# Performance work log

Measured on AMD Instinct MI355X. Metric: run time of the kernel, lower is better.

## Reference

```python
import jax, jax.numpy as jnp
import numpy as np

D_MODEL = 1024
D_FF = 8192
N_ELEM = 64            # d2 (elements per block)
D1 = D_FF // N_ELEM    # 128 block rows
BATCH = 2048


def setup_inputs() -> dict:
    key = jax.random.key(0)
    k1, k2, k3, k4, k5 = jax.random.split(key, 5)
    # xavier-uniform-like init for w1 (d_model, d_ff) -> view (d_model, d1, d2)
    bound1 = float(np.sqrt(6.0 / (D_MODEL + D_FF)))
    w1 = jax.random.uniform(k1, (D_MODEL, D1, N_ELEM), jnp.float32, -bound1, bound1)
    # w2 (d_ff, d_model) -> view (d2, d1, d_model); kernel_scaling=True multiplies by sqrt(d2)
    w2 = jax.random.uniform(k2, (N_ELEM, D1, D_MODEL), jnp.float32, -bound1, bound1)
    w2 = w2 * (N_ELEM ** 0.5)
    b2 = jax.random.normal(k3, (D_MODEL,), jnp.float32)
    x = jax.random.normal(k4, (BATCH, D_MODEL), jnp.float32)
    quant_mask = jax.random.randint(k5, (BATCH, D1), 0, N_ELEM, jnp.int32)
    return {"quant_mask": quant_mask, "x": x, "w1": w1, "w2": w2, "b2": b2}


def reference(quant_mask, x, w1, w2, b2):
    # predict-mode path of SparseFFMain (multiply_by_controller_output=False)
    d1 = w1.shape[1]
    w1p = jnp.transpose(w1, (1, 2, 0))   # (d1, d2, d_model)
    w2p = jnp.transpose(w2, (1, 0, 2))   # (d1, d2, d_model)
    rows = jnp.arange(d1)[None, :]        # (1, d1) broadcasts over batch
    # per-sample gathered expert sub-blocks: (B, d1, d_model)
    w = w1p[rows, quant_mask]
    v = w2p[rows, quant_mask]
    mid = jnp.einsum('bd,bjd->bj', x, w)   # (B, d1)
    relu = jax.nn.relu(mid)
    res = jnp.einsum('bj,bjd->bd', relu, v) + b2  # (B, d_model)
    return (quant_mask, res)
```

## Files before the change

kernel.cpp:

```cpp
#include <hip/hip_runtime.h>

#define D_MODEL 1024
#define D_FF    8192
#define N_ELEM  64
#define D1      128
#define BATCH   2048
#define B_T     8
#define NJT     8
#define JT      16

typedef unsigned short u16;
typedef unsigned int   u32;
typedef _Float16 h2    __attribute__((ext_vector_type(2)));
typedef float    f32x4 __attribute__((ext_vector_type(4)));
typedef u32      u32x2 __attribute__((ext_vector_type(2)));

__device__ __forceinline__ h2 as_h2(u32 u) { union { u32 i; h2 h; } c; c.i = u; return c.h; }
__device__ __forceinline__ u32 pkh(float a, float b) {
    union { h2 h; u32 u; } c; c.h.x = (_Float16)a; c.h.y = (_Float16)b; return c.u;
}
__device__ __forceinline__ u16 f2h(float f) {
    union { _Float16 h; u16 u; } c; c.h = (_Float16)f; return c.u;
}
__device__ __forceinline__ f32x4 ntload4(const float* p) {
    return __builtin_nontemporal_load((const f32x4*)p);
}

__global__ __launch_bounds__(256) void transpose_cast_w1(const float* __restrict__ w1,
                                                         u16* __restrict__ w1h) {
    __shared__ float tile[64][65];
    const int c0 = blockIdx.x * 64;
    const int d0 = blockIdx.y * 64;
    const int tx = threadIdx.x & 15;
    const int ty = threadIdx.x >> 4;
#pragma unroll
    for (int r = 0; r < 4; ++r) {
        const int row = ty * 4 + r;
        const float4 v = *(const float4*)(w1 + (size_t)(d0 + row) * D_FF + c0 + tx * 4);
        tile[row][tx * 4 + 0] = v.x;
        tile[row][tx * 4 + 1] = v.y;
        tile[row][tx * 4 + 2] = v.z;
        tile[row][tx * 4 + 3] = v.w;
    }
    __syncthreads();
#pragma unroll
    for (int r = 0; r < 4; ++r) {
        const int c = ty * 4 + r;
        ushort4 o;
        o.x = f2h(tile[tx * 4 + 0][c]);
        o.y = f2h(tile[tx * 4 + 1][c]);
        o.z = f2h(tile[tx * 4 + 2][c]);
        o.w = f2h(tile[tx * 4 + 3][c]);
        *(ushort4*)(w1h + (size_t)(c0 + c) * D_MODEL + d0 + tx * 4) = o;
    }
}

__global__ __launch_bounds__(256) void cast_w2(const float* __restrict__ w2,
                                               u16* __restrict__ w2h) {
    const size_t i = ((size_t)blockIdx.x * 256 + threadIdx.x) * 8;
    const float4 a = *(const float4*)(w2 + i);
    const float4 b = *(const float4*)(w2 + i + 4);
    ushort4 oa, ob;
    oa.x = f2h(a.x); oa.y = f2h(a.y); oa.z = f2h(a.z); oa.w = f2h(a.w);
    ob.x = f2h(b.x); ob.y = f2h(b.y); ob.z = f2h(b.z); ob.w = f2h(b.w);
    *(ushort4*)(w2h + i)     = oa;
    *(ushort4*)(w2h + i + 4) = ob;
}

__global__ __launch_bounds__(256) void sparse_ff_jt(const int* __restrict__ mask,
                                                    const float* __restrict__ x,
                                                    const u16* __restrict__ w1h_,
                                                    const u16* __restrict__ w2h_,
                                                    u16* __restrict__ part) {
    const _Float16* w1h = (const _Float16*)w1h_;
    const _Float16* w2h = (const _Float16*)w2h_;
    __shared__ u16   x_lds[B_T][D_MODEL];
    __shared__ float r_lds[B_T][JT];
    __shared__ int   m_lds[B_T][JT];

    const int jt = blockIdx.x & (NJT - 1);
    const int b0 = (blockIdx.x >> 3) * B_T;
    const int t = threadIdx.x;
    const int wave = t >> 6;
    const int lane = t & 63;

#pragma unroll
    for (int r = 0; r < B_T; ++r) {
        const f32x4 v = ntload4(x + (size_t)(b0 + r) * D_MODEL + t * 4);
        u32x2 o; o.x = pkh(v.x, v.y); o.y = pkh(v.z, v.w);
        *(u32x2*)&x_lds[r][t * 4] = o;
    }
    if (t < B_T * JT) {
        m_lds[t >> 4][t & 15] = mask[(b0 + (t >> 4)) * D1 + jt * JT + (t & 15)];
    }
    __syncthreads();

#pragma unroll
    for (int rep = 0; rep < 2; ++rep) {
        const int bi = wave * 2 + rep;
        const uint4 xA = *(const uint4*)&x_lds[bi][lane * 8];
        const uint4 xB = *(const uint4*)&x_lds[bi][512 + lane * 8];

        for (int jj = 0; jj < JT; jj += 2) {
            const int j0 = jt * JT + jj;
            const _Float16* c0 = w1h + (size_t)((j0 << 6) + m_lds[bi][jj]) * D_MODEL;
            const _Float16* c1 = w1h + (size_t)(((j0 + 1) << 6) + m_lds[bi][jj + 1]) * D_MODEL;
            const uint4 a0 = *(const uint4*)(c0 + lane * 8);
            const uint4 b0v = *(const uint4*)(c0 + 512 + lane * 8);
            const uint4 a1 = *(const uint4*)(c1 + lane * 8);
            const uint4 b1v = *(const uint4*)(c1 + 512 + lane * 8);

            float s0 = 0.f, s1 = 0.f;
            {
                const h2 w_0 = as_h2(a0.x), w_1 = as_h2(a0.y), w_2 = as_h2(a0.z), w_3 = as_h2(a0.w);
                const h2 q_0 = as_h2(xA.x), q_1 = as_h2(xA.y), q_2 = as_h2(xA.z), q_3 = as_h2(xA.w);
                s0 = fmaf((float)w_0.x, (float)q_0.x, s0); s0 = fmaf((float)w_0.y, (float)q_0.y, s0);
                s0 = fmaf((float)w_1.x, (float)q_1.x, s0); s0 = fmaf((float)w_1.y, (float)q_1.y, s0);
                s0 = fmaf((float)w_2.x, (float)q_2.x, s0); s0 = fmaf((float)w_2.y, (float)q_2.y, s0);
                s0 = fmaf((float)w_3.x, (float)q_3.x, s0); s0 = fmaf((float)w_3.y, (float)q_3.y, s0);
            }
            {
                const h2 w_0 = as_h2(b0v.x), w_1 = as_h2(b0v.y), w_2 = as_h2(b0v.z), w_3 = as_h2(b0v.w);
                const h2 q_0 = as_h2(xB.x), q_1 = as_h2(xB.y), q_2 = as_h2(xB.z), q_3 = as_h2(xB.w);
                s0 = fmaf((float)w_0.x, (float)q_0.x, s0); s0 = fmaf((float)w_0.y, (float)q_0.y, s0);
                s0 = fmaf((float)w_1.x, (float)q_1.x, s0); s0 = fmaf((float)w_1.y, (float)q_1.y, s0);
                s0 = fmaf((float)w_2.x, (float)q_2.x, s0); s0 = fmaf((float)w_2.y, (float)q_2.y, s0);
                s0 = fmaf((float)w_3.x, (float)q_3.x, s0); s0 = fmaf((float)w_3.y, (float)q_3.y, s0);
            }
            {
                const h2 w_0 = as_h2(a1.x), w_1 = as_h2(a1.y), w_2 = as_h2(a1.z), w_3 = as_h2(a1.w);
                const h2 q_0 = as_h2(xA.x), q_1 = as_h2(xA.y), q_2 = as_h2(xA.z), q_3 = as_h2(xA.w);
                s1 = fmaf((float)w_0.x, (float)q_0.x, s1); s1 = fmaf((float)w_0.y, (float)q_0.y, s1);
                s1 = fmaf((float)w_1.x, (float)q_1.x, s1); s1 = fmaf((float)w_1.y, (float)q_1.y, s1);
                s1 = fmaf((float)w_2.x, (float)q_2.x, s1); s1 = fmaf((float)w_2.y, (float)q_2.y, s1);
                s1 = fmaf((float)w_3.x, (float)q_3.x, s1); s1 = fmaf((float)w_3.y, (float)q_3.y, s1);
            }
            {
                const h2 w_0 = as_h2(b1v.x), w_1 = as_h2(b1v.y), w_2 = as_h2(b1v.z), w_3 = as_h2(b1v.w);
                const h2 q_0 = as_h2(xB.x), q_1 = as_h2(xB.y), q_2 = as_h2(xB.z), q_3 = as_h2(xB.w);
                s1 = fmaf((float)w_0.x, (float)q_0.x, s1); s1 = fmaf((float)w_0.y, (float)q_0.y, s1);
                s1 = fmaf((float)w_1.x, (float)q_1.x, s1); s1 = fmaf((float)w_1.y, (float)q_1.y, s1);
                s1 = fmaf((float)w_2.x, (float)q_2.x, s1); s1 = fmaf((float)w_2.y, (float)q_2.y, s1);
                s1 = fmaf((float)w_3.x, (float)q_3.x, s1); s1 = fmaf((float)w_3.y, (float)q_3.y, s1);
            }

#pragma unroll
            for (int off = 32; off; off >>= 1) {
                s0 += __shfl_down(s0, off);
                s1 += __shfl_down(s1, off);
            }
            if (lane == 0) {
                r_lds[bi][jj]     = fmaxf(s0, 0.f);
                r_lds[bi][jj + 1] = fmaxf(s1, 0.f);
            }
        }
    }
    __syncthreads();

    const int d0q = t * 4;
    for (int bi = 0; bi < B_T; ++bi) {
        float a0 = 0.f, a1 = 0.f, a2 = 0.f, a3 = 0.f;
        for (int jj = 0; jj < JT; ++jj) {
            const float r = r_lds[bi][jj];
            if (r > 0.f) {
                const _Float16* row = w2h
                    + (size_t)(m_lds[bi][jj] * D1 + jt * JT + jj) * D_MODEL + d0q;
                const uint2 v = *(const uint2*)row;
                const h2 p0 = as_h2(v.x), p1 = as_h2(v.y);
                a0 = fmaf(r, (float)p0.x, a0); a1 = fmaf(r, (float)p0.y, a1);
                a2 = fmaf(r, (float)p1.x, a2); a3 = fmaf(r, (float)p1.y, a3);
            }
        }
        u32x2 o;
        o.x = pkh(a0, a1);
        o.y = pkh(a2, a3);
        u16* pp = part + ((size_t)jt * BATCH + (b0 + bi)) * D_MODEL + d0q;
        __builtin_nontemporal_store(o, (u32x2*)pp);
    }
}

__global__ __launch_bounds__(256) void reduce_partials(const int* __restrict__ mask,
                                                       const float* __restrict__ b2,
                                                       const u16* __restrict__ part,
                                                       float* __restrict__ out) {
    const int b = blockIdx.x;
    const int t = threadIdx.x;
    if (t < D1) out[(size_t)b * D1 + t] = (float)mask[b * D1 + t];

    const int d0 = t * 4;
    const float4 bv = *(const float4*)(b2 + d0);
    float a0 = bv.x, a1 = bv.y, a2 = bv.z, a3 = bv.w;
#pragma unroll
    for (int jt = 0; jt < NJT; ++jt) {
        const uint2 v = *(const uint2*)(part + ((size_t)jt * BATCH + b) * D_MODEL + d0);
        const h2 p0 = as_h2(v.x), p1 = as_h2(v.y);
        a0 += (float)p0.x; a1 += (float)p0.y;
        a2 += (float)p1.x; a3 += (float)p1.y;
    }
    *(float4*)(out + (size_t)BATCH * D1 + (size_t)b * D_MODEL + d0) =
        make_float4(a0, a1, a2, a3);
}

__global__ __launch_bounds__(256) void sparse_ff_f32_raw(const int* __restrict__ mask,
                                                         const float* __restrict__ x,
                                                         const float* __restrict__ w1,
                                                         const float* __restrict__ w2,
                                                         const float* __restrict__ b2,
                                                         float* __restrict__ out) {
    __shared__ float x_lds[D_MODEL];
    __shared__ float relu_lds[D1];
    __shared__ int   m_lds[D1];
    const int b = blockIdx.x, t = threadIdx.x;
    const int wave = t >> 6, lane = t & 63;
    *(float4*)&x_lds[t * 4] = *(const float4*)(x + (size_t)b * D_MODEL + t * 4);
    if (t < D1) {
        const int mv = mask[b * D1 + t];
        m_lds[t] = mv;
        out[(size_t)b * D1 + t] = (float)mv;
    }
    __syncthreads();
    for (int jj = 0; jj < 32; ++jj) {
        const int j = wave * 32 + jj;
        const int m = m_lds[j];
        float acc = 0.f;
#pragma unroll
        for (int c = 0; c < 16; ++c) {
            const int d = c * 64 + lane;
            acc = fmaf(w1[(size_t)d * D_FF + j * N_ELEM + m], x_lds[d], acc);
        }
#pragma unroll
        for (int off = 32; off; off >>= 1) acc += __shfl_down(acc, off);
        if (lane == 0) relu_lds[j] = fmaxf(acc, 0.f);
    }
    __syncthreads();
    const int dm0 = t * 4;
    const float4 bv = *(const float4*)(b2 + dm0);
    float a0 = bv.x, a1 = bv.y, a2 = bv.z, a3 = bv.w;
    for (int j = 0; j < D1; ++j) {
        const float r = relu_lds[j];
        if (r > 0.f) {
            const float4 wv = *(const float4*)(w2 + (size_t)(m_lds[j] * D1 + j) * D_MODEL + dm0);
            a0 = fmaf(r, wv.x, a0); a1 = fmaf(r, wv.y, a1);
            a2 = fmaf(r, wv.z, a2); a3 = fmaf(r, wv.w, a3);
        }
    }
    *(float4*)(out + (size_t)BATCH * D1 + (size_t)b * D_MODEL + dm0) =
        make_float4(a0, a1, a2, a3);
}

extern "C" void kernel_launch(void* const* d_in, const int* in_sizes, int n_in,
                              void* d_out, int out_size, void* d_ws, size_t ws_size,
                              hipStream_t stream) {
    const int*   mask = (const int*)d_in[0];
    const float* x    = (const float*)d_in[1];
    const float* w1   = (const float*)d_in[2];
    const float* w2   = (const float*)d_in[3];
    const float* b2   = (const float*)d_in[4];
    float* out = (float*)d_out;

    const size_t w1h_bytes  = (size_t)D_FF * D_MODEL * sizeof(u16);
    const size_t w2h_bytes  = (size_t)D_FF * D_MODEL * sizeof(u16);
    const size_t part_bytes = (size_t)NJT * BATCH * D_MODEL * sizeof(u16);

    if (ws_size >= w1h_bytes + w2h_bytes + part_bytes) {
        u16* w1h  = (u16*)d_ws;
        u16* w2h  = (u16*)((char*)d_ws + w1h_bytes);
        u16* part = (u16*)((char*)d_ws + w1h_bytes + w2h_bytes);
        transpose_cast_w1<<<dim3(D_FF / 64, D_MODEL / 64), 256, 0, stream>>>(w1, w1h);
        cast_w2<<<(D_FF * D_MODEL / 8) / 256, 256, 0, stream>>>(w2, w2h);
        sparse_ff_jt<<<(BATCH / B_T) * NJT, 256, 0, stream>>>(mask, x, w1h, w2h, part);
        reduce_partials<<<BATCH, 256, 0, stream>>>(mask, b2, part, out);
    } else {
        sparse_ff_f32_raw<<<BATCH, 256, 0, stream>>>(mask, x, w1, w2, b2, out);
    }
}
```

Measured before the change: 183.5 us.

## Merge weight prep kernels and restructure sparse FF dot products with fdot2

Fuses the w1 transpose-cast and w2 cast into one launch. Restructures the first stage so each 16-lane group handles four j rows with 16-byte loads, using packed fp16 dot2 instructions and a shorter 16-lane shuffle reduction. The second stage now has each thread produce 8 outputs with wider loads and stores, with the mask value made wave-uniform via readfirstlane. Adds an occupancy hint to launch_bounds. The aim is fewer instructions, fewer launches and more memory-level parallelism, at the cost of higher register pressure.

```diff
diff --git a/kernel.cpp b/kernel.cpp
--- a/kernel.cpp
+++ b/kernel.cpp
@@ -14,6 +14,7 @@
 typedef _Float16 h2    __attribute__((ext_vector_type(2)));
 typedef float    f32x4 __attribute__((ext_vector_type(4)));
 typedef u32      u32x2 __attribute__((ext_vector_type(2)));
+typedef u32      u32x4 __attribute__((ext_vector_type(4)));
 
 __device__ __forceinline__ h2 as_h2(u32 u) { union { u32 i; h2 h; } c; c.i = u; return c.h; }
 __device__ __forceinline__ u32 pkh(float a, float b) {
@@ -25,53 +26,64 @@
 __device__ __forceinline__ f32x4 ntload4(const float* p) {
     return __builtin_nontemporal_load((const f32x4*)p);
 }
-
-__global__ __launch_bounds__(256) void transpose_cast_w1(const float* __restrict__ w1,
-                                                         u16* __restrict__ w1h) {
+__device__ __forceinline__ float dot2(u32 a, u32 b, float c) {
+#if __has_builtin(__builtin_amdgcn_fdot2)
+    return __builtin_amdgcn_fdot2(as_h2(a), as_h2(b), c, false);
+#else
+    const h2 ha = as_h2(a), hb = as_h2(b);
+    c = fmaf((float)ha.x, (float)hb.x, c);
+    return fmaf((float)ha.y, (float)hb.y, c);
+#endif
+}
+
+#define TW1_BLOCKS ((D_FF / 64) * (D_MODEL / 64))
+__global__ __launch_bounds__(256) void prep_weights(const float* __restrict__ w1,
+                                                    u16* __restrict__ w1h,
+                                                    const float* __restrict__ w2,
+                                                    u16* __restrict__ w2h) {
     __shared__ float tile[64][65];
-    const int c0 = blockIdx.x * 64;
-    const int d0 = blockIdx.y * 64;
-    const int tx = threadIdx.x & 15;
-    const int ty = threadIdx.x >> 4;
-#pragma unroll
-    for (int r = 0; r < 4; ++r) {
-        const int row = ty * 4 + r;
-        const float4 v = *(const float4*)(w1 + (size_t)(d0 + row) * D_FF + c0 + tx * 4);
-        tile[row][tx * 4 + 0] = v.x;
-        tile[row][tx * 4 + 1] = v.y;
-        tile[row][tx * 4 + 2] = v.z;
-        tile[row][tx * 4 + 3] = v.w;
-    }
-    __syncthreads();
-#pragma unroll
-    for (int r = 0; r < 4; ++r) {
-        const int c = ty * 4 + r;
-        ushort4 o;
-        o.x = f2h(tile[tx * 4 + 0][c]);
-        o.y = f2h(tile[tx * 4 + 1][c]);
-        o.z = f2h(tile[tx * 4 + 2][c]);
-        o.w = f2h(tile[tx * 4 + 3][c]);
-        *(ushort4*)(w1h + (size_t)(c0 + c) * D_MODEL + d0 + tx * 4) = o;
-    }
-}
-
-__global__ __launch_bounds__(256) void cast_w2(const float* __restrict__ w2,
-                                               u16* __restrict__ w2h) {
-    const size_t i = ((size_t)blockIdx.x * 256 + threadIdx.x) * 8;
-    const float4 a = *(const float4*)(w2 + i);
-    const float4 b = *(const float4*)(w2 + i + 4);
-    ushort4 oa, ob;
-    oa.x = f2h(a.x); oa.y = f2h(a.y); oa.z = f2h(a.z); oa.w = f2h(a.w);
-    ob.x = f2h(b.x); ob.y = f2h(b.y); ob.z = f2h(b.z); ob.w = f2h(b.w);
-    *(ushort4*)(w2h + i)     = oa;
-    *(ushort4*)(w2h + i + 4) = ob;
-}
-
-__global__ __launch_bounds__(256) void sparse_ff_jt(const int* __restrict__ mask,
-                                                    const float* __restrict__ x,
-                                                    const u16* __restrict__ w1h_,
-                                                    const u16* __restrict__ w2h_,
-                                                    u16* __restrict__ part) {
+    if (blockIdx.x < TW1_BLOCKS) {
+        const int c0 = (blockIdx.x & (D_FF / 64 - 1)) * 64;
+        const int d0 = (blockIdx.x >> 7) * 64;
+        const int tx = threadIdx.x & 15;
+        const int ty = threadIdx.x >> 4;
+#pragma unroll
+        for (int r = 0; r < 4; ++r) {
+            const int row = ty * 4 + r;
+            const float4 v = *(const float4*)(w1 + (size_t)(d0 + row) * D_FF + c0 + tx * 4);
+            tile[row][tx * 4 + 0] = v.x;
+            tile[row][tx * 4 + 1] = v.y;
+            tile[row][tx * 4 + 2] = v.z;
+            tile[row][tx * 4 + 3] = v.w;
+        }
+        __syncthreads();
+#pragma unroll
+        for (int r = 0; r < 4; ++r) {
+            const int c = ty * 4 + r;
+            ushort4 o;
+            o.x = f2h(tile[tx * 4 + 0][c]);
+            o.y = f2h(tile[tx * 4 + 1][c]);
+            o.z = f2h(tile[tx * 4 + 2][c]);
+            o.w = f2h(tile[tx * 4 + 3][c]);
+            *(ushort4*)(w1h + (size_t)(c0 + c) * D_MODEL + d0 + tx * 4) = o;
+        }
+    } else {
+        const size_t i = ((size_t)(blockIdx.x - TW1_BLOCKS) * 256 + threadIdx.x) * 8;
+        const float4 a = *(const float4*)(w2 + i);
+        const float4 b = *(const float4*)(w2 + i + 4);
+        ushort4 oa, ob;
+        oa.x = f2h(a.x); oa.y = f2h(a.y); oa.z = f2h(a.z); oa.w = f2h(a.w);
+        ob.x = f2h(b.x); ob.y = f2h(b.y); ob.z = f2h(b.z); ob.w = f2h(b.w);
+        *(ushort4*)(w2h + i)     = oa;
+        *(ushort4*)(w2h + i + 4) = ob;
+    }
+}
+
+__global__ __launch_bounds__(256, 6) void sparse_ff_jt(const int* __restrict__ mask,
+                                                       const float* __restrict__ x,
+                                                       const u16* __restrict__ w1h_,
+                                                       const u16* __restrict__ w2h_,
+                                                       u16* __restrict__ part) {
     const _Float16* w1h = (const _Float16*)w1h_;
     const _Float16* w2h = (const _Float16*)w2h_;
     __shared__ u16   x_lds[B_T][D_MODEL];
@@ -83,6 +95,8 @@
     const int t = threadIdx.x;
     const int wave = t >> 6;
     const int lane = t & 63;
+    const int q = lane >> 4;
+    const int l = lane & 15;
 
 #pragma unroll
     for (int r = 0; r < B_T; ++r) {
@@ -98,84 +112,79 @@
 #pragma unroll
     for (int rep = 0; rep < 2; ++rep) {
         const int bi = wave * 2 + rep;
-        const uint4 xA = *(const uint4*)&x_lds[bi][lane * 8];
-        const uint4 xB = *(const uint4*)&x_lds[bi][512 + lane * 8];
-
-        for (int jj = 0; jj < JT; jj += 2) {
-            const int j0 = jt * JT + jj;
-            const _Float16* c0 = w1h + (size_t)((j0 << 6) + m_lds[bi][jj]) * D_MODEL;
-            const _Float16* c1 = w1h + (size_t)(((j0 + 1) << 6) + m_lds[bi][jj + 1]) * D_MODEL;
-            const uint4 a0 = *(const uint4*)(c0 + lane * 8);
-            const uint4 b0v = *(const uint4*)(c0 + 512 + lane * 8);
-            const uint4 a1 = *(const uint4*)(c1 + lane * 8);
-            const uint4 b1v = *(const uint4*)(c1 + 512 + lane * 8);
-
-            float s0 = 0.f, s1 = 0.f;
-            {
-                const h2 w_0 = as_h2(a0.x), w_1 = as_h2(a0.y), w_2 = as_h2(a0.z), w_3 = as_h2(a0.w);
-                const h2 q_0 = as_h2(xA.x), q_1 = as_h2(xA.y), q_2 = as_h2(xA.z), q_3 = as_h2(xA.w);
-                s0 = fmaf((float)w_0.x, (float)q_0.x, s0); s0 = fmaf((float)w_0.y, (float)q_0.y, s0);
-                s0 = fmaf((float)w_1.x, (float)q_1.x, s0); s0 = fmaf((float)w_1.y, (float)q_1.y, s0);
-                s0 = fmaf((float)w_2.x, (float)q_2.x, s0); s0 = fmaf((float)w_2.y, (float)q_2.y, s0);
-                s0 = fmaf((float)w_3.x, (float)q_3.x, s0); s0 = fmaf((float)w_3.y, (float)q_3.y, s0);
+        const int4 mv = *(const int4*)&m_lds[bi][q * 4];
+        const int mj[4] = {mv.x, mv.y, mv.z, mv.w};
+        float sj[4] = {0.f, 0.f, 0.f, 0.f};
+#pragma unroll
+        for (int half = 0; half < 2; ++half) {
+            uint4 xv[4];
+#pragma unroll
+            for (int i = 0; i < 4; ++i)
+                xv[i] = *(const uint4*)&x_lds[bi][half * 512 + i * 128 + l * 8];
+#pragma unroll
+            for (int jg = 0; jg < 4; ++jg) {
+                const int j0 = jt * JT + q * 4 + jg;
+                const _Float16* row =
+                    w1h + (size_t)((j0 << 6) + mj[jg]) * D_MODEL + half * 512 + l * 8;
+                uint4 wv[4];
+#pragma unroll
+                for (int i = 0; i < 4; ++i)
+                    wv[i] = *(const uint4*)(row + i * 128);
+#pragma unroll
+                for (int i = 0; i < 4; ++i) {
+                    sj[jg] = dot2(wv[i].x, xv[i].x, sj[jg]);
+                    sj[jg] = dot2(wv[i].y, xv[i].y, sj[jg]);
+                    sj[jg] = dot2(wv[i].z, xv[i].z, sj[jg]);
+                    sj[jg] = dot2(wv[i].w, xv[i].w, sj[jg]);
+                }
             }
-            {
-                const h2 w_0 = as_h2(b0v.x), w_1 = as_h2(b0v.y), w_2 = as_h2(b0v.z), w_3 = as_h2(b0v.w);
-                const h2 q_0 = as_h2(xB.x), q_1 = as_h2(xB.y), q_2 = as_h2(xB.z), q_3 = as_h2(xB.w);
-                s0 = fmaf((float)w_0.x, (float)q_0.x, s0); s0 = fmaf((float)w_0.y, (float)q_0.y, s0);
-                s0 = fmaf((float)w_1.x, (float)q_1.x, s0); s0 = fmaf((float)w_1.y, (float)q_1.y, s0);
-                s0 = fmaf((float)w_2.x, (float)q_2.x, s0); s0 = fmaf((float)w_2.y, (float)q_2.y, s0);
-                s0 = fmaf((float)w_3.x, (float)q_3.x, s0); s0 = fmaf((float)w_3.y, (float)q_3.y, s0);
+        }
+#pragma unroll
+        for (int jg = 0; jg < 4; ++jg) {
+            float s = sj[jg];
+            s += __shfl_down(s, 8, 16);
+            s += __shfl_down(s, 4, 16);
+            s += __shfl_down(s, 2, 16);
+            s += __shfl_down(s, 1, 16);
+            if (l == 0) r_lds[bi][q * 4 + jg] = fmaxf(s, 0.f);
+        }
+    }
+    __syncthreads();
+
+    const int halfsel = t >> 7;
+    const int d0q = (t & 127) * 8;
+#pragma unroll
+    for (int p = 0; p < 4; ++p) {
+        const int bi = p * 2 + halfsel;
+        float rr[16];
+        int   mm[16];
+#pragma unroll
+        for (int i = 0; i < 4; ++i) {
+            *(float4*)&rr[i * 4] = *(const float4*)&r_lds[bi][i * 4];
+            *(int4*)&mm[i * 4]   = *(const int4*)&m_lds[bi][i * 4];
+        }
+        float a[8] = {0.f, 0.f, 0.f, 0.f, 0.f, 0.f, 0.f, 0.f};
+#pragma unroll
+        for (int jj = 0; jj < JT; ++jj) {
+            const float r = rr[jj];
+            if (r > 0.f) {
+                const int m = __builtin_amdgcn_readfirstlane(mm[jj]);
+                const _Float16* row =
+                    w2h + (size_t)(m * D1 + jt * JT + jj) * D_MODEL + d0q;
+                const uint4 v = *(const uint4*)row;
+                const h2 p0 = as_h2(v.x), p1 = as_h2(v.y);
+                const h2 p2 = as_h2(v.z), p3 = as_h2(v.w);
+                a[0] = fmaf(r, (float)p0.x, a[0]); a[1] = fmaf(r, (float)p0.y, a[1]);
+                a[2] = fmaf(r, (float)p1.x, a[2]); a[3] = fmaf(r, (float)p1.y, a[3]);
+                a[4] = fmaf(r, (float)p2.x, a[4]); a[5] = fmaf(r, (float)p2.y, a[5]);
+                a[6] = fmaf(r, (float)p3.x, a[6]); a[7] = fmaf(r, (float)p3.y, a[7]);
             }
-            {
-                const h2 w_0 = as_h2(a1.x), w_1 = as_h2(a1.y), w_2 = as_h2(a1.z), w_3 = as_h2(a1.w);
-                const h2 q_0 = as_h2(xA.x), q_1 = as_h2(xA.y), q_2 = as_h2(xA.z), q_3 = as_h2(xA.w);
-                s1 = fmaf((float)w_0.x, (float)q_0.x, s1); s1 = fmaf((float)w_0.y, (float)q_0.y, s1);
-                s1 = fmaf((float)w_1.x, (float)q_1.x, s1); s1 = fmaf((float)w_1.y, (float)q_1.y, s1);
-                s1 = fmaf((float)w_2.x, (float)q_2.x, s1); s1 = fmaf((float)w_2.y, (float)q_2.y, s1);
-                s1 = fmaf((float)w_3.x, (float)q_3.x, s1); s1 = fmaf((float)w_3.y, (float)q_3.y, s1);
-            }
-            {
-                const h2 w_0 = as_h2(b1v.x), w_1 = as_h2(b1v.y), w_2 = as_h2(b1v.z), w_3 = as_h2(b1v.w);
-                const h2 q_0 = as_h2(xB.x), q_1 = as_h2(xB.y), q_2 = as_h2(xB.z), q_3 = as_h2(xB.w);
-                s1 = fmaf((float)w_0.x, (float)q_0.x, s1); s1 = fmaf((float)w_0.y, (float)q_0.y, s1);
-                s1 = fmaf((float)w_1.x, (float)q_1.x, s1); s1 = fmaf((float)w_1.y, (float)q_1.y, s1);
-                s1 = fmaf((float)w_2.x, (float)q_2.x, s1); s1 = fmaf((float)w_2.y, (float)q_2.y, s1);
-                s1 = fmaf((float)w_3.x, (float)q_3.x, s1); s1 = fmaf((float)w_3.y, (float)q_3.y, s1);
-            }
-
-#pragma unroll
-            for (int off = 32; off; off >>= 1) {
-                s0 += __shfl_down(s0, off);
-                s1 += __shfl_down(s1, off);
-            }
-            if (lane == 0) {
-                r_lds[bi][jj]     = fmaxf(s0, 0.f);
-                r_lds[bi][jj + 1] = fmaxf(s1, 0.f);
-            }
-        }
-    }
-    __syncthreads();
-
-    const int d0q = t * 4;
-    for (int bi = 0; bi < B_T; ++bi) {
-        float a0 = 0.f, a1 = 0.f, a2 = 0.f, a3 = 0.f;
-        for (int jj = 0; jj < JT; ++jj) {
-            const float r = r_lds[bi][jj];
-            if (r > 0.f) {
-                const _Float16* row = w2h
-                    + (size_t)(m_lds[bi][jj] * D1 + jt * JT + jj) * D_MODEL + d0q;
-                const uint2 v = *(const uint2*)row;
-                const h2 p0 = as_h2(v.x), p1 = as_h2(v.y);
-                a0 = fmaf(r, (float)p0.x, a0); a1 = fmaf(r, (float)p0.y, a1);
-                a2 = fmaf(r, (float)p1.x, a2); a3 = fmaf(r, (float)p1.y, a3);
-            }
-        }
-        u32x2 o;
-        o.x = pkh(a0, a1);
-        o.y = pkh(a2, a3);
+        }
+        u32x4 o;
+        o.x = pkh(a[0], a[1]); o.y = pkh(a[2], a[3]);
+        o.z = pkh(a[4], a[5]); o.w = pkh(a[6], a[7]);
         u16* pp = part + ((size_t)jt * BATCH + (b0 + bi)) * D_MODEL + d0q;
-        __builtin_nontemporal_store(o, (u32x2*)pp);
+        __builtin_nontemporal_store(o, (u32x4*)pp);
     }
 }
 
@@ -266,8 +275,8 @@
         u16* w1h  = (u16*)d_ws;
         u16* w2h  = (u16*)((char*)d_ws + w1h_bytes);
         u16* part = (u16*)((char*)d_ws + w1h_bytes + w2h_bytes);
-        transpose_cast_w1<<<dim3(D_FF / 64, D_MODEL / 64), 256, 0, stream>>>(w1, w1h);
-        cast_w2<<<(D_FF * D_MODEL / 8) / 256, 256, 0, stream>>>(w2, w2h);
+        const int cast_blocks = (D_FF * D_MODEL / 8) / 256;
+        prep_weights<<<TW1_BLOCKS + cast_blocks, 256, 0, stream>>>(w1, w1h, w2, w2h);
         sparse_ff_jt<<<(BATCH / B_T) * NJT, 256, 0, stream>>>(mask, x, w1h, w2h, part);
         reduce_partials<<<BATCH, 256, 0, stream>>>(mask, b2, part, out);
     } else {
```

Result: slower. 282.0 us (+53.7%).

## Merge weight prep kernels, prefetch w1 rows, use fdot2 for dot products

Applied to the files above, without the earlier changes.

Fuses the w1 transpose-cast and w2 cast into one launch so a kernel boundary and its tail idle time go away. In the main kernel, the next pair of gathered w1 rows is loaded before the current pair is computed, which hides global load latency through software pipelining. The per-element fp16-to-fp32 converts plus FMAs are replaced with the packed fdot2 instruction, which cuts ALU work. The trade-off is more registers held live for the prefetch, and a slightly different accumulation order from fdot2.

```diff
diff --git a/kernel.cpp b/kernel.cpp
--- a/kernel.cpp
+++ b/kernel.cpp
@@ -25,46 +25,64 @@
 __device__ __forceinline__ f32x4 ntload4(const float* p) {
     return __builtin_nontemporal_load((const f32x4*)p);
 }
-
-__global__ __launch_bounds__(256) void transpose_cast_w1(const float* __restrict__ w1,
-                                                         u16* __restrict__ w1h) {
+__device__ __forceinline__ float dot2(u32 a, u32 b, float c) {
+#if __has_builtin(__builtin_amdgcn_fdot2)
+    return __builtin_amdgcn_fdot2(as_h2(a), as_h2(b), c, false);
+#else
+    const h2 ha = as_h2(a), hb = as_h2(b);
+    c = fmaf((float)ha.x, (float)hb.x, c);
+    return fmaf((float)ha.y, (float)hb.y, c);
+#endif
+}
+__device__ __forceinline__ float dot8(uint4 w, uint4 q, float c) {
+    c = dot2(w.x, q.x, c);
+    c = dot2(w.y, q.y, c);
+    c = dot2(w.z, q.z, c);
+    c = dot2(w.w, q.w, c);
+    return c;
+}
+
+#define TW1_BLOCKS ((D_FF / 64) * (D_MODEL / 64))
+__global__ __launch_bounds__(256) void prep_weights(const float* __restrict__ w1,
+                                                    u16* __restrict__ w1h,
+                                                    const float* __restrict__ w2,
+                                                    u16* __restrict__ w2h) {
     __shared__ float tile[64][65];
-    const int c0 = blockIdx.x * 64;
-    const int d0 = blockIdx.y * 64;
-    const int tx = threadIdx.x & 15;
-    const int ty = threadIdx.x >> 4;
-#pragma unroll
-    for (int r = 0; r < 4; ++r) {
-        const int row = ty * 4 + r;
-        const float4 v = *(const float4*)(w1 + (size_t)(d0 + row) * D_FF + c0 + tx * 4);
-        tile[row][tx * 4 + 0] = v.x;
-        tile[row][tx * 4 + 1] = v.y;
-        tile[row][tx * 4 + 2] = v.z;
-        tile[row][tx * 4 + 3] = v.w;
-    }
-    __syncthreads();
-#pragma unroll
-    for (int r = 0; r < 4; ++r) {
-        const int c = ty * 4 + r;
-        ushort4 o;
-        o.x = f2h(tile[tx * 4 + 0][c]);
-        o.y = f2h(tile[tx * 4 + 1][c]);
-        o.z = f2h(tile[tx * 4 + 2][c]);
-        o.w = f2h(tile[tx * 4 + 3][c]);
-        *(ushort4*)(w1h + (size_t)(c0 + c) * D_MODEL + d0 + tx * 4) = o;
-    }
-}
-
-__global__ __launch_bounds__(256) void cast_w2(const float* __restrict__ w2,
-                                               u16* __restrict__ w2h) {
-    const size_t i = ((size_t)blockIdx.x * 256 + threadIdx.x) * 8;
-    const float4 a = *(const float4*)(w2 + i);
-    const float4 b = *(const float4*)(w2 + i + 4);
-    ushort4 oa, ob;
-    oa.x = f2h(a.x); oa.y = f2h(a.y); oa.z = f2h(a.z); oa.w = f2h(a.w);
-    ob.x = f2h(b.x); ob.y = f2h(b.y); ob.z = f2h(b.z); ob.w = f2h(b.w);
-    *(ushort4*)(w2h + i)     = oa;
-    *(ushort4*)(w2h + i + 4) = ob;
+    if (blockIdx.x < TW1_BLOCKS) {
+        const int c0 = (blockIdx.x & (D_FF / 64 - 1)) * 64;
+        const int d0 = (blockIdx.x >> 7) * 64;
+        const int tx = threadIdx.x & 15;
+        const int ty = threadIdx.x >> 4;
+#pragma unroll
+        for (int r = 0; r < 4; ++r) {
+            const int row = ty * 4 + r;
+            const float4 v = *(const float4*)(w1 + (size_t)(d0 + row) * D_FF + c0 + tx * 4);
+            tile[row][tx * 4 + 0] = v.x;
+            tile[row][tx * 4 + 1] = v.y;
+            tile[row][tx * 4 + 2] = v.z;
+            tile[row][tx * 4 + 3] = v.w;
+        }
+        __syncthreads();
+#pragma unroll
+        for (int r = 0; r < 4; ++r) {
+            const int c = ty * 4 + r;
+            ushort4 o;
+            o.x = f2h(tile[tx * 4 + 0][c]);
+            o.y = f2h(tile[tx * 4 + 1][c]);
+            o.z = f2h(tile[tx * 4 + 2][c]);
+            o.w = f2h(tile[tx * 4 + 3][c]);
+            *(ushort4*)(w1h + (size_t)(c0 + c) * D_MODEL + d0 + tx * 4) = o;
+        }
+    } else {
+        const size_t i = ((size_t)(blockIdx.x - TW1_BLOCKS) * 256 + threadIdx.x) * 8;
+        const float4 a = *(const float4*)(w2 + i);
+        const float4 b = *(const float4*)(w2 + i + 4);
+        ushort4 oa, ob;
+        oa.x = f2h(a.x); oa.y = f2h(a.y); oa.z = f2h(a.z); oa.w = f2h(a.w);
+        ob.x = f2h(b.x); ob.y = f2h(b.y); ob.z = f2h(b.z); ob.w = f2h(b.w);
+        *(ushort4*)(w2h + i)     = oa;
+        *(ushort4*)(w2h + i + 4) = ob;
+    }
 }
 
 __global__ __launch_bounds__(256) void sparse_ff_jt(const int* __restrict__ mask,
@@ -101,48 +119,31 @@
         const uint4 xA = *(const uint4*)&x_lds[bi][lane * 8];
         const uint4 xB = *(const uint4*)&x_lds[bi][512 + lane * 8];
 
+        const _Float16* p0 = w1h + (size_t)(((jt * JT) << 6) + m_lds[bi][0]) * D_MODEL;
+        const _Float16* p1 = w1h + (size_t)((((jt * JT) + 1) << 6) + m_lds[bi][1]) * D_MODEL;
+        uint4 a0  = *(const uint4*)(p0 + lane * 8);
+        uint4 b0v = *(const uint4*)(p0 + 512 + lane * 8);
+        uint4 a1  = *(const uint4*)(p1 + lane * 8);
+        uint4 b1v = *(const uint4*)(p1 + 512 + lane * 8);
+
+#pragma unroll
         for (int jj = 0; jj < JT; jj += 2) {
-            const int j0 = jt * JT + jj;
-            const _Float16* c0 = w1h + (size_t)((j0 << 6) + m_lds[bi][jj]) * D_MODEL;
-            const _Float16* c1 = w1h + (size_t)(((j0 + 1) << 6) + m_lds[bi][jj + 1]) * D_MODEL;
-            const uint4 a0 = *(const uint4*)(c0 + lane * 8);
-            const uint4 b0v = *(const uint4*)(c0 + 512 + lane * 8);
-            const uint4 a1 = *(const uint4*)(c1 + lane * 8);
-            const uint4 b1v = *(const uint4*)(c1 + 512 + lane * 8);
+            uint4 na0, nb0, na1, nb1;
+            if (jj + 2 < JT) {
+                const int j0 = jt * JT + jj + 2;
+                const _Float16* c0 = w1h + (size_t)((j0 << 6) + m_lds[bi][jj + 2]) * D_MODEL;
+                const _Float16* c1 = w1h + (size_t)(((j0 + 1) << 6) + m_lds[bi][jj + 3]) * D_MODEL;
+                na0 = *(const uint4*)(c0 + lane * 8);
+                nb0 = *(const uint4*)(c0 + 512 + lane * 8);
+                na1 = *(const uint4*)(c1 + lane * 8);
+                nb1 = *(const uint4*)(c1 + 512 + lane * 8);
+            }
 
             float s0 = 0.f, s1 = 0.f;
-            {
-                const h2 w_0 = as_h2(a0.x), w_1 = as_h2(a0.y), w_2 = as_h2(a0.z), w_3 = as_h2(a0.w);
-                const h2 q_0 = as_h2(xA.x), q_1 = as_h2(xA.y), q_2 = as_h2(xA.z), q_3 = as_h2(xA.w);
-                s0 = fmaf((float)w_0.x, (float)q_0.x, s0); s0 = fmaf((float)w_0.y, (float)q_0.y, s0);
-                s0 = fmaf((float)w_1.x, (float)q_1.x, s0); s0 = fmaf((float)w_1.y, (float)q_1.y, s0);
-                s0 = fmaf((float)w_2.x, (float)q_2.x, s0); s0 = fmaf((float)w_2.y, (float)q_2.y, s0);
-                s0 = fmaf((float)w_3.x, (float)q_3.x, s0); s0 = fmaf((float)w_3.y, (float)q_3.y, s0);
-            }
-            {
-                const h2 w_0 = as_h2(b0v.x), w_1 = as_h2(b0v.y), w_2 = as_h2(b0v.z), w_3 = as_h2(b0v.w);
-                const h2 q_0 = as_h2(xB.x), q_1 = as_h2(xB.y), q_2 = as_h2(xB.z), q_3 = as_h2(xB.w);
-                s0 = fmaf((float)w_0.x, (float)q_0.x, s0); s0 = fmaf((float)w_0.y, (float)q_0.y, s0);
-                s0 = fmaf((float)w_1.x, (float)q_1.x, s0); s0 = fmaf((float)w_1.y, (float)q_1.y, s0);
-                s0 = fmaf((float)w_2.x, (float)q_2.x, s0); s0 = fmaf((float)w_2.y, (float)q_2.y, s0);
-                s0 = fmaf((float)w_3.x, (float)q_3.x, s0); s0 = fmaf((float)w_3.y, (float)q_3.y, s0);
-            }
-            {
-                const h2 w_0 = as_h2(a1.x), w_1 = as_h2(a1.y), w_2 = as_h2(a1.z), w_3 = as_h2(a1.w);
-                const h2 q_0 = as_h2(xA.x), q_1 = as_h2(xA.y), q_2 = as_h2(xA.z), q_3 = as_h2(xA.w);
-                s1 = fmaf((float)w_0.x, (float)q_0.x, s1); s1 = fmaf((float)w_0.y, (float)q_0.y, s1);
-                s1 = fmaf((float)w_1.x, (float)q_1.x, s1); s1 = fmaf((float)w_1.y, (float)q_1.y, s1);
-                s1 = fmaf((float)w_2.x, (float)q_2.x, s1); s1 = fmaf((float)w_2.y, (float)q_2.y, s1);
-                s1 = fmaf((float)w_3.x, (float)q_3.x, s1); s1 = fmaf((float)w_3.y, (float)q_3.y, s1);
-            }
-            {
-                const h2 w_0 = as_h2(b1v.x), w_1 = as_h2(b1v.y), w_2 = as_h2(b1v.z), w_3 = as_h2(b1v.w);
-                const h2 q_0 = as_h2(xB.x), q_1 = as_h2(xB.y), q_2 = as_h2(xB.z), q_3 = as_h2(xB.w);
-                s1 = fmaf((float)w_0.x, (float)q_0.x, s1); s1 = fmaf((float)w_0.y, (float)q_0.y, s1);
-                s1 = fmaf((float)w_1.x, (float)q_1.x, s1); s1 = fmaf((float)w_1.y, (float)q_1.y, s1);
-                s1 = fmaf((float)w_2.x, (float)q_2.x, s1); s1 = fmaf((float)w_2.y, (float)q_2.y, s1);
-                s1 = fmaf((float)w_3.x, (float)q_3.x, s1); s1 = fmaf((float)w_3.y, (float)q_3.y, s1);
-            }
+            s0 = dot8(a0, xA, s0);
+            s0 = dot8(b0v, xB, s0);
+            s1 = dot8(a1, xA, s1);
+            s1 = dot8(b1v, xB, s1);
 
 #pragma unroll
             for (int off = 32; off; off >>= 1) {
@@ -153,6 +154,7 @@
                 r_lds[bi][jj]     = fmaxf(s0, 0.f);
                 r_lds[bi][jj + 1] = fmaxf(s1, 0.f);
             }
+            a0 = na0; b0v = nb0; a1 = na1; b1v = nb1;
         }
     }
     __syncthreads();
@@ -166,9 +168,9 @@
                 const _Float16* row = w2h
                     + (size_t)(m_lds[bi][jj] * D1 + jt * JT + jj) * D_MODEL + d0q;
                 const uint2 v = *(const uint2*)row;
-                const h2 p0 = as_h2(v.x), p1 = as_h2(v.y);
-                a0 = fmaf(r, (float)p0.x, a0); a1 = fmaf(r, (float)p0.y, a1);
-                a2 = fmaf(r, (float)p1.x, a2); a3 = fmaf(r, (float)p1.y, a3);
+                const h2 q0 = as_h2(v.x), q1 = as_h2(v.y);
+                a0 = fmaf(r, (float)q0.x, a0); a1 = fmaf(r, (float)q0.y, a1);
+                a2 = fmaf(r, (float)q1.x, a2); a3 = fmaf(r, (float)q1.y, a3);
             }
         }
         u32x2 o;
@@ -266,8 +268,8 @@
         u16* w1h  = (u16*)d_ws;
         u16* w2h  = (u16*)((char*)d_ws + w1h_bytes);
         u16* part = (u16*)((char*)d_ws + w1h_bytes + w2h_bytes);
-        transpose_cast_w1<<<dim3(D_FF / 64, D_MODEL / 64), 256, 0, stream>>>(w1, w1h);
-        cast_w2<<<(D_FF * D_MODEL / 8) / 256, 256, 0, stream>>>(w2, w2h);
+        const int cast_blocks = (D_FF * D_MODEL / 8) / 256;
+        prep_weights<<<TW1_BLOCKS + cast_blocks, 256, 0, stream>>>(w1, w1h, w2, w2h);
         sparse_ff_jt<<<(BATCH / B_T) * NJT, 256, 0, stream>>>(mask, x, w1h, w2h, part);
         reduce_partials<<<BATCH, 256, 0, stream>>>(mask, b2, part, out);
     } else {
```

Measured after the change: 181.0 us. About the same (-1.4%).
